# Performance work log

Hardware: AMD Instinct MI355X
Metric: run time of the kernel (lower is better)

Reference implementation:

```python
import jax, jax.numpy as jnp
import numpy as np

N_NODES = 100000
N_EDGES = 1600000
N_GRAPHS = 4096
IN_FEATS = 64
HIDDEN = 128


def setup_inputs() -> dict:
    key = jax.random.key(0)
    ks = jax.random.split(key, 16)
    feats_node = jax.random.normal(ks[0], (N_NODES, IN_FEATS), dtype=jnp.float32)
    feats_graph = jax.random.normal(ks[1], (N_GRAPHS, 3), dtype=jnp.float32)
    src = jax.random.randint(ks[2], (N_EDGES,), 0, N_NODES, dtype=jnp.int32)
    dst = jax.random.randint(ks[3], (N_EDGES,), 0, N_NODES, dtype=jnp.int32)
    node2graph = jnp.sort(jax.random.randint(ks[4], (N_NODES,), 0, N_GRAPHS, dtype=jnp.int32))
    # weights stored as [in, out] (torch Linear W.T); init per module: std=0.5 weights, bias ~ N(0.01, 0.001)
    def w(k, shape):
        return jax.random.normal(k, shape, dtype=jnp.float32) * 0.5
    def b(k, shape):
        return 0.01 + 0.001 * jax.random.normal(k, shape, dtype=jnp.float32)
    return {
        'feats_node': feats_node, 'feats_graph': feats_graph,
        'src': src, 'dst': dst, 'node2graph': node2graph,
        'W1': w(ks[5], (IN_FEATS, HIDDEN)), 'b1': b(ks[6], (HIDDEN,)),
        'W2': w(ks[7], (HIDDEN, HIDDEN)), 'b2': b(ks[8], (HIDDEN,)),
        'W3': w(ks[9], (HIDDEN, HIDDEN)), 'b3': b(ks[10], (HIDDEN,)),
        'L1w': w(ks[11], (HIDDEN + 3, 2 * HIDDEN)), 'L1b': b(ks[12], (2 * HIDDEN,)),
        'L2w': w(ks[13], (2 * HIDDEN, HIDDEN)), 'L2b': b(ks[14], (HIDDEN,)),
        'L3w': w(ks[15], (HIDDEN, 1)), 'L3b': b(jax.random.fold_in(key, 99), (1,)),
    }


def _graph_conv(x, W, b, src, dst, norm_out, norm_in):
    # DGL GraphConv(norm='both'): h_i = (sum_{j->i} x_j * d_out(j)^-1/2) * d_in(i)^-1/2 @ W + b
    m = (x * norm_out)[src]                       # [E, F] gather
    agg = jax.ops.segment_sum(m, dst, num_segments=N_NODES)
    return (agg * norm_in) @ W + b


def reference(feats_node, feats_graph, W1, b1, W2, b2, W3, b3, L1w, L1b, L2w, L2b, L3w, L3b, src, dst, node2graph):
    ones = jnp.ones((N_EDGES,), dtype=jnp.float32)
    deg_out = jax.ops.segment_sum(ones, src, num_segments=N_NODES)
    deg_in = jax.ops.segment_sum(ones, dst, num_segments=N_NODES)
    norm_out = jnp.clip(deg_out, 1.0, None)[:, None] ** -0.5  # [N,1]
    norm_in = jnp.clip(deg_in, 1.0, None)[:, None] ** -0.5

    x = jax.nn.selu(_graph_conv(feats_node, W1, b1, src, dst, norm_out, norm_in))
    x = jax.nn.selu(_graph_conv(x, W2, b2, src, dst, norm_out, norm_in))
    y_node = _graph_conv(x, W3, b3, src, dst, norm_out, norm_in)

    y_sum = jax.ops.segment_sum(y_node, node2graph, num_segments=N_GRAPHS)  # readout 'sum'
    y = jnp.concatenate([y_sum, feats_graph], axis=1)  # [G, H+3]
    y = jax.nn.selu(y @ L1w + L1b)
    y = jax.nn.selu(y @ L2w + L2b)
    return (y @ L3w + L3b).reshape(-1)
```

## Files before the change

### kernel.cpp

```cpp
#include <hip/hip_runtime.h>
#include <math.h>

#define SELU_ALPHA 1.6732632423543772f
#define SELU_SCALE 1.0507009873554805f

#define NBLK 512
#define MAXBKT 512

typedef __attribute__((ext_vector_type(8))) short bf16x8;
typedef __attribute__((ext_vector_type(4))) float f32x4;

__device__ __forceinline__ float selu_f(float x) {
    return SELU_SCALE * (x > 0.f ? x : SELU_ALPHA * expm1f(x));
}

__device__ __forceinline__ float bf2f(unsigned short u) {
    return __uint_as_float(((unsigned)u) << 16);
}
__device__ __forceinline__ unsigned short f2bf(float f) {
    unsigned u = __float_as_uint(f);
    unsigned r = (u + 0x7fffu + ((u >> 16) & 1u)) >> 16;
    return (unsigned short)r;
}

#define SCAN_B 1024

__global__ __launch_bounds__(256) void scan_block_sums(const int* __restrict__ in,
                                                       int* __restrict__ bsums, int n) {
    __shared__ int s[256];
    int b = blockIdx.x, t = threadIdx.x;
    int base = b * SCAN_B;
    int sum = 0;
    for (int i = t; i < SCAN_B; i += 256) {
        int idx = base + i;
        sum += (idx < n) ? in[idx] : 0;
    }
    s[t] = sum; __syncthreads();
    for (int off = 128; off > 0; off >>= 1) {
        if (t < off) s[t] += s[t + off];
        __syncthreads();
    }
    if (t == 0) bsums[b] = s[0];
}

__global__ __launch_bounds__(256) void scan_apply2(const int* __restrict__ in,
                                                   const int* __restrict__ bsums,
                                                   int* __restrict__ out, int n, int nb) {
    __shared__ int sb[512];
    __shared__ int s[256];
    __shared__ int blockoff;
    int b = blockIdx.x, t = threadIdx.x;

    int orig0 = (t < nb) ? bsums[t] : 0;
    int orig1 = (t + 256 < nb) ? bsums[t + 256] : 0;
    sb[t] = orig0; sb[t + 256] = orig1;
    __syncthreads();
    for (int off = 1; off < 512; off <<= 1) {
        int v0 = (t >= off) ? sb[t - off] : 0;
        int v1 = (t + 256 >= off) ? sb[t + 256 - off] : 0;
        __syncthreads();
        sb[t] += v0; sb[t + 256] += v1;
        __syncthreads();
    }
    if (t == (b & 255)) {
        bool hi = b >= 256;
        int incl = hi ? sb[t + 256] : sb[t];
        int orig = hi ? orig1 : orig0;
        blockoff = incl - orig;
    }
    __syncthreads();

    int idx0 = b * SCAN_B + t * 4;
    int v[4]; int tsum = 0;
    #pragma unroll
    for (int k = 0; k < 4; ++k) {
        int idx = idx0 + k;
        v[k] = (idx < n) ? in[idx] : 0;
        tsum += v[k];
    }
    s[t] = tsum; __syncthreads();
    for (int off = 1; off < 256; off <<= 1) {
        int x = (t >= off) ? s[t - off] : 0;
        __syncthreads();
        s[t] += x;
        __syncthreads();
    }
    int run = s[t] - tsum + blockoff;
    #pragma unroll
    for (int k = 0; k < 4; ++k) {
        int idx = idx0 + k;
        if (idx < n) out[idx] = run;
        run += v[k];
    }
}

__global__ __launch_bounds__(256) void hist_prep_kernel(
        const int* __restrict__ src, const int* __restrict__ dst,
        int* __restrict__ cntD, int* __restrict__ cntS, int E, int nbkt,
        const float* __restrict__ W1, const float* __restrict__ W2,
        const float* __restrict__ W3, const float* __restrict__ L1w,
        const float* __restrict__ L2w,
        unsigned short* __restrict__ Wt1, unsigned short* __restrict__ Wt2,
        unsigned short* __restrict__ Wt3, unsigned short* __restrict__ L1w16,
        unsigned short* __restrict__ L2w16) {
    if (blockIdx.x >= NBLK) {
        const int s0 = 128 * 64, s1 = 128 * 128, s2 = 128 * 128;
        const int s3 = 131 * 256 / 4, s4 = 256 * 128 / 4;
        int i = (blockIdx.x - NBLK) * 256 + threadIdx.x;
        if (i < s0) { int col = i / 64, k = i % 64; Wt1[i] = f2bf(W1[k * 128 + col]); return; }
        i -= s0;
        if (i < s1) { int col = i / 128, k = i % 128; Wt2[i] = f2bf(W2[k * 128 + col]); return; }
        i -= s1;
        if (i < s2) { int col = i / 128, k = i % 128; Wt3[i] = f2bf(W3[k * 128 + col]); return; }
        i -= s2;
        if (i < s3) {
            float4 v = reinterpret_cast<const float4*>(L1w)[i];
            unsigned short o[4] = { f2bf(v.x), f2bf(v.y), f2bf(v.z), f2bf(v.w) };
            reinterpret_cast<uint2*>(L1w16)[i] = *reinterpret_cast<uint2*>(o);
            return;
        }
        i -= s3;
        if (i < s4) {
            float4 v = reinterpret_cast<const float4*>(L2w)[i];
            unsigned short o[4] = { f2bf(v.x), f2bf(v.y), f2bf(v.z), f2bf(v.w) };
            reinterpret_cast<uint2*>(L2w16)[i] = *reinterpret_cast<uint2*>(o);
        }
        return;
    }
    __shared__ int hD[MAXBKT];
    __shared__ int hS[MAXBKT];
    int bb = blockIdx.x, t = threadIdx.x;
    for (int k = t; k < MAXBKT; k += 256) { hD[k] = 0; hS[k] = 0; }
    __syncthreads();
    int chunk = E / NBLK;
    int beg = bb * chunk, end = beg + chunk;
    for (int i = beg + t; i < end; i += 256) {
        atomicAdd(&hD[((unsigned)dst[i]) >> 8], 1);
        atomicAdd(&hS[((unsigned)src[i]) >> 8], 1);
    }
    __syncthreads();
    for (int k = t; k < nbkt; k += 256) {
        cntD[k * NBLK + bb] = hD[k];
        cntS[k * NBLK + bb] = hS[k];
    }
}

__global__ __launch_bounds__(256) void scatter_kernel(
        const int* __restrict__ src, const int* __restrict__ dst,
        const int* __restrict__ cntD, const int* __restrict__ cntS,
        unsigned* __restrict__ pairs, int* __restrict__ sbufm, int E, int nbkt) {
    __shared__ int cD[MAXBKT];
    __shared__ int cS[MAXBKT];
    int bb = blockIdx.x, t = threadIdx.x;
    for (int k = t; k < nbkt; k += 256) {
        cD[k] = cntD[k * NBLK + bb];
        cS[k] = cntS[k * NBLK + bb];
    }
    __syncthreads();
    int chunk = E / NBLK;
    int beg = bb * chunk, end = beg + chunk;
    for (int i = beg + t; i < end; i += 256) {
        unsigned s = (unsigned)src[i], d = (unsigned)dst[i];
        int pD = atomicAdd(&cD[d >> 8], 1);
        pairs[pD] = s | ((d & 255u) << 24);
        int pS = atomicAdd(&cS[s >> 8], 1);
        sbufm[pS] = (int)s;
    }
}

__global__ __launch_bounds__(256) void bucket_build_kernel(
        const int* __restrict__ sbufm, const unsigned* __restrict__ pairs,
        const int* __restrict__ cntD, const int* __restrict__ cntS,
        const float* __restrict__ feats,
        float* __restrict__ norm_out, unsigned short* __restrict__ feats16,
        int* __restrict__ row_start, int* __restrict__ deg_in,
        int* __restrict__ csr_src, int N, int E, int nbkt) {
    __shared__ int hist[256];
    __shared__ int sc[256];
    __shared__ int cur[256];
    __shared__ float nrm[256];
    int b = blockIdx.x, t = threadIdx.x;
    int node = (b << 8) + t;
    int node0 = b << 8;

    {
        int base = cntS[b * NBLK];
        int end = (b + 1 < nbkt) ? cntS[(b + 1) * NBLK] : 2 * E;
        hist[t] = 0; __syncthreads();
        for (int i = base + t; i < end; i += 256)
            atomicAdd(&hist[sbufm[i] & 255], 1);
        __syncthreads();
        float no = 1.f / sqrtf(fmaxf((float)hist[t], 1.f));
        nrm[t] = no;
        if (node < N) norm_out[node] = no;
        __syncthreads();
    }

    {
        int cnt = min(256, N - node0);
        for (int i = t; i < cnt * 8; i += 256) {
            int nl = i >> 3, c = i & 7;
            float no = nrm[nl];
            const float* fp = feats + (size_t)(node0 + nl) * 64 + c * 8;
            float4 a = *reinterpret_cast<const float4*>(fp);
            float4 bv = *reinterpret_cast<const float4*>(fp + 4);
            unsigned short o[8] = { f2bf(a.x * no), f2bf(a.y * no), f2bf(a.z * no), f2bf(a.w * no),
                                    f2bf(bv.x * no), f2bf(bv.y * no), f2bf(bv.z * no), f2bf(bv.w * no) };
            *reinterpret_cast<float4*>(feats16 + (size_t)(node0 + nl) * 64 + c * 8) =
                *reinterpret_cast<float4*>(o);
        }
        __syncthreads();
    }

    {
        int base = cntD[b * NBLK];
        int end = (b + 1 < nbkt) ? cntD[(b + 1) * NBLK] : E;
        hist[t] = 0; __syncthreads();
        for (int i = base + t; i < end; i += 256)
            atomicAdd(&hist[(pairs[i] >> 24) & 255], 1);
        __syncthreads();
        int v = hist[t];
        sc[t] = v; __syncthreads();
        for (int off = 1; off < 256; off <<= 1) {
            int x = (t >= off) ? sc[t - off] : 0;
            __syncthreads();
            sc[t] += x;
            __syncthreads();
        }
        int ex = sc[t] - v;
        cur[t] = base + ex;
        if (node < N) { row_start[node] = base + ex; deg_in[node] = v; }
        __syncthreads();
        for (int i = base + t; i < end; i += 256) {
            unsigned p = pairs[i];
            int pos = atomicAdd(&cur[(p >> 24) & 255], 1);
            csr_src[pos] = (int)(p & 0xFFFFFFu);
        }
    }
}

template<int TPG, int FIN>
__global__ __launch_bounds__(256) void csr_agg_kernel(
        const unsigned short* __restrict__ x, const int* __restrict__ row_start,
        const int* __restrict__ deg_in, const int* __restrict__ csr_src,
        unsigned short* __restrict__ agg, int N) {
    const int GPB = 256 / TPG;
    int g = threadIdx.x / TPG;
    int j = threadIdx.x % TPG;
    int n = blockIdx.x * GPB + g;
    if (n >= N) return;
    const int lane = threadIdx.x & 63;
    const int gbase = lane & ~(TPG - 1);
    int beg = row_start[n];
    int dg = deg_in[n];
    int end = beg + dg;
    float nin = 1.f / sqrtf(fmaxf((float)dg, 1.f));
    float acc[8] = {0.f, 0.f, 0.f, 0.f, 0.f, 0.f, 0.f, 0.f};
    int myIdx = (beg + j < end) ? csr_src[beg + j] : 0;
    for (int c = beg; c < end; c += TPG) {
        int cnt = end - c;
        int nxtIdx = (c + TPG + j < end) ? csr_src[c + TPG + j] : 0;
        float4 v[TPG];
        #pragma unroll
        for (int t = 0; t < TPG; ++t) {
            if (t < cnt) {
                int s = __shfl(myIdx, gbase + t, 64);
                v[t] = *reinterpret_cast<const float4*>(&x[(size_t)s * FIN + j * 8]);
            }
        }
        #pragma unroll
        for (int t = 0; t < TPG; ++t) {
            if (t < cnt) {
                const unsigned short* u = reinterpret_cast<const unsigned short*>(&v[t]);
                #pragma unroll
                for (int k = 0; k < 8; ++k) acc[k] += bf2f(u[k]);
            }
        }
        myIdx = nxtIdx;
    }
    unsigned short ov[8];
    #pragma unroll
    for (int k = 0; k < 8; ++k) ov[k] = f2bf(acc[k] * nin);
    *reinterpret_cast<float4*>(&agg[(size_t)n * FIN + j * 8]) = *reinterpret_cast<float4*>(ov);
}

template<int FIN, bool SELU, bool SCALE_OUT>
__global__ __launch_bounds__(256, 4) void gemm_mfma_kernel(
        const unsigned short* __restrict__ agg16,
        const unsigned short* __restrict__ Wt,
        const float* __restrict__ b,
        const float* __restrict__ norm_out,
        unsigned short* __restrict__ out,
        int N) {
    const int PAD = 8;
    const int LDW = FIN + PAD;
    const int CH = FIN / 8;
    __shared__ unsigned short sW[128 * LDW];
    const int tid = threadIdx.x;
    const int wave = tid >> 6, lane = tid & 63;
    const int wr = (wave >> 1) * 64;
    const int wc = (wave & 1) * 64;
    const int n0 = blockIdx.x * 128;

    for (int i = tid; i < 128 * CH; i += 256) {
        int col = i / CH, kc = i % CH;
        *reinterpret_cast<float4*>(&sW[col * LDW + kc * 8]) =
            *reinterpret_cast<const float4*>(&Wt[col * FIN + kc * 8]);
    }
    __syncthreads();

    const int l16 = lane & 15;
    const int lk = (lane >> 4) * 8;
    const bf16x8 zero8 = (bf16x8){0,0,0,0,0,0,0,0};
    f32x4 acc[4][4];
    #pragma unroll
    for (int mi = 0; mi < 4; ++mi)
        #pragma unroll
        for (int ci = 0; ci < 4; ++ci)
            acc[mi][ci] = (f32x4){0.f, 0.f, 0.f, 0.f};

    #pragma unroll
    for (int k0 = 0; k0 < FIN; k0 += 32) {
        bf16x8 a[4], w[4];
        #pragma unroll
        for (int mi = 0; mi < 4; ++mi) {
            int n = n0 + wr + mi * 16 + l16;
            a[mi] = (n < N)
                ? *reinterpret_cast<const bf16x8*>(&agg16[(size_t)n * FIN + k0 + lk])
                : zero8;
        }
        #pragma unroll
        for (int ci = 0; ci < 4; ++ci)
            w[ci] = *reinterpret_cast<const bf16x8*>(&sW[(wc + ci * 16 + l16) * LDW + k0 + lk]);
        #pragma unroll
        for (int mi = 0; mi < 4; ++mi)
            #pragma unroll
            for (int ci = 0; ci < 4; ++ci)
                acc[mi][ci] = __builtin_amdgcn_mfma_f32_16x16x32_bf16(
                    a[mi], w[ci], acc[mi][ci], 0, 0, 0);
    }

    const int rbase = (lane >> 4) * 4;
    #pragma unroll
    for (int ci = 0; ci < 4; ++ci) {
        int col = wc + ci * 16 + l16;
        float bias = b[col];
        #pragma unroll
        for (int mi = 0; mi < 4; ++mi) {
            #pragma unroll
            for (int r = 0; r < 4; ++r) {
                int n = n0 + wr + mi * 16 + rbase + r;
                if (n < N) {
                    float v = acc[mi][ci][r] + bias;
                    if (SELU) v = selu_f(v);
                    if (SCALE_OUT) v *= norm_out[n];
                    out[(size_t)n * 128 + col] = f2bf(v);
                }
            }
        }
    }
}

__global__ __launch_bounds__(128) void readout_kernel(
        const unsigned short* __restrict__ y, const int* __restrict__ n2g,
        float* __restrict__ gsum, int N, int G) {
    int g = blockIdx.x;
    int o = threadIdx.x;
    if (g >= G) return;
    int beg, end;
    {
        int lo = 0, hi = N;
        while (lo < hi) { int m = (lo + hi) >> 1; if (n2g[m] < g) lo = m + 1; else hi = m; }
        beg = lo;
        lo = beg; hi = N;
        while (lo < hi) { int m = (lo + hi) >> 1; if (n2g[m] < g + 1) lo = m + 1; else hi = m; }
        end = lo;
    }
    float acc = 0.f;
    for (int n = beg; n < end; ++n)
        acc += bf2f(y[(size_t)n * 128 + o]);
    gsum[(size_t)g * 128 + o] = acc;
}

__global__ __launch_bounds__(256) void mlp1_kernel(
        const float* __restrict__ gsum, const float* __restrict__ fg,
        const unsigned short* __restrict__ W16,
        const float* __restrict__ b,
        float* __restrict__ y1, int G) {
    __shared__ unsigned short sW[131 * 256];
    __shared__ float sIn[16][132];
    int tid = threadIdx.x;
    for (int i = tid; i < 131 * 256 / 2; i += 256)
        reinterpret_cast<unsigned*>(sW)[i] = reinterpret_cast<const unsigned*>(W16)[i];
    int g0 = blockIdx.x * 16;
    for (int i = tid; i < 16 * 131; i += 256) {
        int g = i / 131, k = i - g * 131;
        float v = 0.f;
        if (g0 + g < G)
            v = (k < 128) ? gsum[(size_t)(g0 + g) * 128 + k]
                          : fg[(size_t)(g0 + g) * 3 + (k - 128)];
        sIn[g][k] = v;
    }
    __syncthreads();
    float bias = b[tid];
    for (int g = 0; g < 16; ++g) {
        if (g0 + g >= G) break;
        float acc = bias;
        #pragma unroll 8
        for (int k = 0; k < 131; ++k)
            acc += sIn[g][k] * bf2f(sW[k * 256 + tid]);
        y1[(size_t)(g0 + g) * 256 + tid] = selu_f(acc);
    }
}

__global__ __launch_bounds__(256) void mlp23_kernel(
        const float* __restrict__ y1,
        const unsigned short* __restrict__ W16,
        const float* __restrict__ b2v,
        const float* __restrict__ L3w,
        const float* __restrict__ L3b,
        float* __restrict__ out, int G) {
    __shared__ unsigned short sW[256 * 128];
    __shared__ float sIn[16][256];
    __shared__ float sL3[128];
    __shared__ float red[16][2];
    int tid = threadIdx.x;
    for (int i = tid; i < 256 * 128 / 2; i += 256)
        reinterpret_cast<unsigned*>(sW)[i] = reinterpret_cast<const unsigned*>(W16)[i];
    if (tid < 128) sL3[tid] = L3w[tid];
    int g0 = blockIdx.x * 16;
    for (int i = tid; i < 16 * 256; i += 256) {
        int g = i >> 8, k = i & 255;
        sIn[g][k] = (g0 + g < G) ? y1[(size_t)(g0 + g) * 256 + k] : 0.f;
    }
    __syncthreads();
    int o = tid & 127;
    int half = tid >> 7;
    int lane = tid & 63;
    int wv = tid >> 6;
    float bias = b2v[o];
    float w3 = sL3[o];
    for (int gg = 0; gg < 8; ++gg) {
        int g = half * 8 + gg;
        float acc = bias;
        #pragma unroll 8
        for (int k = 0; k < 256; ++k)
            acc += sIn[g][k] * bf2f(sW[k * 128 + o]);
        float v = selu_f(acc) * w3;
        #pragma unroll
        for (int off = 32; off > 0; off >>= 1)
            v += __shfl_down(v, off, 64);
        if (lane == 0) red[g][wv & 1] = v;
    }
    __syncthreads();
    if (tid < 16) {
        int g = g0 + tid;
        if (g < G) out[g] = red[tid][0] + red[tid][1] + L3b[0];
    }
}

extern "C" void kernel_launch(void* const* d_in, const int* in_sizes, int n_in,
                              void* d_out, int out_size, void* d_ws, size_t ws_size,
                              hipStream_t stream) {
    const float* feats_node  = (const float*)d_in[0];
    const float* feats_graph = (const float*)d_in[1];
    const int*   src         = (const int*)d_in[2];
    const int*   dst         = (const int*)d_in[3];
    const int*   node2graph  = (const int*)d_in[4];
    const float* W1 = (const float*)d_in[5];
    const float* b1 = (const float*)d_in[6];
    const float* W2 = (const float*)d_in[7];
    const float* b2 = (const float*)d_in[8];
    const float* W3 = (const float*)d_in[9];
    const float* b3 = (const float*)d_in[10];
    const float* L1w = (const float*)d_in[11];
    const float* L1b = (const float*)d_in[12];
    const float* L2w = (const float*)d_in[13];
    const float* L2b = (const float*)d_in[14];
    const float* L3w = (const float*)d_in[15];
    const float* L3b = (const float*)d_in[16];

    const int N = in_sizes[0] / 64;
    const int G = in_sizes[1] / 3;
    const int E = in_sizes[2];
    const int NBKT = (N + 255) >> 8;
    const int nmat = NBKT * NBLK;
    const int nscan = 2 * nmat;
    const int NBsc = (nscan + SCAN_B - 1) / SCAN_B;

    int* iws = (int*)d_ws;
    int* deg_in_i  = iws;
    int* row_start = deg_in_i + N;
    int* bsums     = row_start + N;
    int* cntD      = bsums + 512;
    int* cntS      = cntD + nmat;
    int* csr_src   = cntS + nmat;

    float* norm_out = (float*)(csr_src + E);

    unsigned short* feats16 = (unsigned short*)(norm_out + N);
    unsigned short* x16     = feats16 + (size_t)N * 64;
    unsigned short* agg16   = x16 + (size_t)N * 128;
    unsigned short* y16     = agg16 + (size_t)N * 128;
    unsigned short* Wt1     = y16 + (size_t)N * 128;
    unsigned short* Wt2     = Wt1 + 128 * 64;
    unsigned short* Wt3     = Wt2 + 128 * 128;
    unsigned short* L1w16   = Wt3 + 128 * 128;
    unsigned short* L2w16   = L1w16 + 131 * 256;

    float* gsum = (float*)(L2w16 + 256 * 128);
    float* y1   = gsum + (size_t)G * 128;

    unsigned* pairs = (unsigned*)(((uintptr_t)y16 + 15) & ~(uintptr_t)15);
    int*      sbuf  = (int*)(pairs + E);
    int*      sbufm = sbuf - E;

    float* out = (float*)d_out;

    {
        const int wtotal = 128 * 64 + 2 * 128 * 128 + 131 * 256 / 4 + 256 * 128 / 4;
        const int wblocks = (wtotal + 255) / 256;
        hist_prep_kernel<<<NBLK + wblocks, 256, 0, stream>>>(
            src, dst, cntD, cntS, E, NBKT,
            W1, W2, W3, L1w, L2w, Wt1, Wt2, Wt3, L1w16, L2w16);
    }

    scan_block_sums<<<NBsc, 256, 0, stream>>>(cntD, bsums, nscan);
    scan_apply2<<<NBsc, 256, 0, stream>>>(cntD, bsums, cntD, nscan, NBsc);
    scatter_kernel<<<NBLK, 256, 0, stream>>>(src, dst, cntD, cntS, pairs, sbufm, E, NBKT);

    bucket_build_kernel<<<NBKT, 256, 0, stream>>>(
        sbufm, pairs, cntD, cntS, feats_node,
        norm_out, feats16, row_start, deg_in_i, csr_src, N, E, NBKT);

    const int gemm_grid = (N + 127) / 128;

    csr_agg_kernel<8, 64><<<(N + 31) / 32, 256, 0, stream>>>(
        feats16, row_start, deg_in_i, csr_src, agg16, N);
    gemm_mfma_kernel<64, true, true><<<gemm_grid, 256, 0, stream>>>(
        agg16, Wt1, b1, norm_out, x16, N);

    csr_agg_kernel<16, 128><<<(N + 15) / 16, 256, 0, stream>>>(
        x16, row_start, deg_in_i, csr_src, agg16, N);
    gemm_mfma_kernel<128, true, true><<<gemm_grid, 256, 0, stream>>>(
        agg16, Wt2, b2, norm_out, x16, N);

    csr_agg_kernel<16, 128><<<(N + 15) / 16, 256, 0, stream>>>(
        x16, row_start, deg_in_i, csr_src, agg16, N);
    gemm_mfma_kernel<128, false, false><<<gemm_grid, 256, 0, stream>>>(
        agg16, Wt3, b3, norm_out, y16, N);

    readout_kernel<<<G, 128, 0, stream>>>(y16, node2graph, gsum, N, G);

    mlp1_kernel<<<(G + 15) / 16, 256, 0, stream>>>(gsum, feats_graph, L1w16, L1b, y1, G);
    mlp23_kernel<<<(G + 15) / 16, 256, 0, stream>>>(
        y1, L2w16, L2b, L3w, L3b, out, G);
}
```

Baseline: 416.9 us.

## Fold layer-3 weight and bias into the first MLP layer algebraically

The third graph-conv layer has no activation before the sum readout and the first MLP linear layer, so W3 is folded into L1w and b3 is turned into a per-graph node-count term. The layer-3 GEMM over all nodes is removed, and readout sums the normalized aggregate directly. In exchange, prep does a small 128x128x256 matmul and the weights and agg16 are rounded to bf16 at different points, which can shift numerics slightly.

```diff
diff --git a/kernel.cpp b/kernel.cpp
--- a/kernel.cpp
+++ b/kernel.cpp
@@ -98,29 +98,49 @@
         const int* __restrict__ src, const int* __restrict__ dst,
         int* __restrict__ cntD, int* __restrict__ cntS, int E, int nbkt,
         const float* __restrict__ W1, const float* __restrict__ W2,
-        const float* __restrict__ W3, const float* __restrict__ L1w,
-        const float* __restrict__ L2w,
+        const float* __restrict__ W3, const float* __restrict__ b3,
+        const float* __restrict__ L1w, const float* __restrict__ L2w,
         unsigned short* __restrict__ Wt1, unsigned short* __restrict__ Wt2,
-        unsigned short* __restrict__ Wt3, unsigned short* __restrict__ L1w16,
-        unsigned short* __restrict__ L2w16) {
+        unsigned short* __restrict__ W1c, unsigned short* __restrict__ L2w16) {
     if (blockIdx.x >= NBLK) {
-        const int s0 = 128 * 64, s1 = 128 * 128, s2 = 128 * 128;
-        const int s3 = 131 * 256 / 4, s4 = 256 * 128 / 4;
+        const int s0 = 128 * 64;
+        const int s1 = 128 * 128;
+        const int s2 = 128 * 256;
+        const int s3 = 3 * 256;
+        const int s4 = 256;
+        const int s5 = 256 * 128 / 4;
         int i = (blockIdx.x - NBLK) * 256 + threadIdx.x;
         if (i < s0) { int col = i / 64, k = i % 64; Wt1[i] = f2bf(W1[k * 128 + col]); return; }
         i -= s0;
         if (i < s1) { int col = i / 128, k = i % 128; Wt2[i] = f2bf(W2[k * 128 + col]); return; }
         i -= s1;
-        if (i < s2) { int col = i / 128, k = i % 128; Wt3[i] = f2bf(W3[k * 128 + col]); return; }
+        if (i < s2) {
+            int k = i >> 8, o = i & 255;
+            float acc = 0.f;
+            #pragma unroll 8
+            for (int m = 0; m < 128; ++m)
+                acc += W3[k * 128 + m] * L1w[m * 256 + o];
+            W1c[k * 256 + o] = f2bf(acc);
+            return;
+        }
         i -= s2;
         if (i < s3) {
-            float4 v = reinterpret_cast<const float4*>(L1w)[i];
-            unsigned short o[4] = { f2bf(v.x), f2bf(v.y), f2bf(v.z), f2bf(v.w) };
-            reinterpret_cast<uint2*>(L1w16)[i] = *reinterpret_cast<uint2*>(o);
+            int r = i >> 8, o = i & 255;
+            W1c[(128 + r) * 256 + o] = f2bf(L1w[(128 + r) * 256 + o]);
             return;
         }
         i -= s3;
         if (i < s4) {
+            int o = i;
+            float acc = 0.f;
+            #pragma unroll 8
+            for (int m = 0; m < 128; ++m)
+                acc += b3[m] * L1w[m * 256 + o];
+            W1c[131 * 256 + o] = f2bf(acc);
+            return;
+        }
+        i -= s4;
+        if (i < s5) {
             float4 v = reinterpret_cast<const float4*>(L2w)[i];
             unsigned short o[4] = { f2bf(v.x), f2bf(v.y), f2bf(v.z), f2bf(v.w) };
             reinterpret_cast<uint2*>(L2w16)[i] = *reinterpret_cast<uint2*>(o);
@@ -363,7 +383,7 @@
 
 __global__ __launch_bounds__(128) void readout_kernel(
         const unsigned short* __restrict__ y, const int* __restrict__ n2g,
-        float* __restrict__ gsum, int N, int G) {
+        float* __restrict__ gsum, float* __restrict__ cntf, int N, int G) {
     int g = blockIdx.x;
     int o = threadIdx.x;
     if (g >= G) return;
@@ -380,25 +400,29 @@
     for (int n = beg; n < end; ++n)
         acc += bf2f(y[(size_t)n * 128 + o]);
     gsum[(size_t)g * 128 + o] = acc;
+    if (o == 0) cntf[g] = (float)(end - beg);
 }
 
 __global__ __launch_bounds__(256) void mlp1_kernel(
         const float* __restrict__ gsum, const float* __restrict__ fg,
-        const unsigned short* __restrict__ W16,
+        const float* __restrict__ cntf,
+        const unsigned short* __restrict__ W1c,
         const float* __restrict__ b,
         float* __restrict__ y1, int G) {
-    __shared__ unsigned short sW[131 * 256];
+    __shared__ unsigned short sW[132 * 256];
     __shared__ float sIn[16][132];
     int tid = threadIdx.x;
-    for (int i = tid; i < 131 * 256 / 2; i += 256)
-        reinterpret_cast<unsigned*>(sW)[i] = reinterpret_cast<const unsigned*>(W16)[i];
+    for (int i = tid; i < 132 * 256 / 2; i += 256)
+        reinterpret_cast<unsigned*>(sW)[i] = reinterpret_cast<const unsigned*>(W1c)[i];
     int g0 = blockIdx.x * 16;
-    for (int i = tid; i < 16 * 131; i += 256) {
-        int g = i / 131, k = i - g * 131;
+    for (int i = tid; i < 16 * 132; i += 256) {
+        int g = i / 132, k = i - g * 132;
         float v = 0.f;
-        if (g0 + g < G)
-            v = (k < 128) ? gsum[(size_t)(g0 + g) * 128 + k]
-                          : fg[(size_t)(g0 + g) * 3 + (k - 128)];
+        if (g0 + g < G) {
+            if (k < 128)       v = gsum[(size_t)(g0 + g) * 128 + k];
+            else if (k < 131)  v = fg[(size_t)(g0 + g) * 3 + (k - 128)];
+            else               v = cntf[g0 + g];
+        }
         sIn[g][k] = v;
     }
     __syncthreads();
@@ -406,8 +430,8 @@
     for (int g = 0; g < 16; ++g) {
         if (g0 + g >= G) break;
         float acc = bias;
-        #pragma unroll 8
-        for (int k = 0; k < 131; ++k)
+        #pragma unroll 4
+        for (int k = 0; k < 132; ++k)
             acc += sIn[g][k] * bf2f(sW[k * 256 + tid]);
         y1[(size_t)(g0 + g) * 256 + tid] = selu_f(acc);
     }
@@ -501,28 +525,27 @@
     unsigned short* feats16 = (unsigned short*)(norm_out + N);
     unsigned short* x16     = feats16 + (size_t)N * 64;
     unsigned short* agg16   = x16 + (size_t)N * 128;
-    unsigned short* y16     = agg16 + (size_t)N * 128;
-    unsigned short* Wt1     = y16 + (size_t)N * 128;
+    unsigned short* Wt1     = agg16 + (size_t)N * 128;
     unsigned short* Wt2     = Wt1 + 128 * 64;
-    unsigned short* Wt3     = Wt2 + 128 * 128;
-    unsigned short* L1w16   = Wt3 + 128 * 128;
-    unsigned short* L2w16   = L1w16 + 131 * 256;
+    unsigned short* W1c     = Wt2 + 128 * 128;
+    unsigned short* L2w16   = W1c + 132 * 256;
 
     float* gsum = (float*)(L2w16 + 256 * 128);
-    float* y1   = gsum + (size_t)G * 128;
-
-    unsigned* pairs = (unsigned*)(((uintptr_t)y16 + 15) & ~(uintptr_t)15);
+    float* cntf = gsum + (size_t)G * 128;
+    float* y1   = cntf + G;
+
+    unsigned* pairs = (unsigned*)(((uintptr_t)agg16 + 15) & ~(uintptr_t)15);
     int*      sbuf  = (int*)(pairs + E);
     int*      sbufm = sbuf - E;
 
     float* out = (float*)d_out;
 
     {
-        const int wtotal = 128 * 64 + 2 * 128 * 128 + 131 * 256 / 4 + 256 * 128 / 4;
+        const int wtotal = 128 * 64 + 128 * 128 + 128 * 256 + 3 * 256 + 256 + 256 * 128 / 4;
         const int wblocks = (wtotal + 255) / 256;
         hist_prep_kernel<<<NBLK + wblocks, 256, 0, stream>>>(
             src, dst, cntD, cntS, E, NBKT,
-            W1, W2, W3, L1w, L2w, Wt1, Wt2, Wt3, L1w16, L2w16);
+            W1, W2, W3, b3, L1w, L2w, Wt1, Wt2, W1c, L2w16);
     }
 
     scan_block_sums<<<NBsc, 256, 0, stream>>>(cntD, bsums, nscan);
@@ -547,12 +570,11 @@
 
     csr_agg_kernel<16, 128><<<(N + 15) / 16, 256, 0, stream>>>(
         x16, row_start, deg_in_i, csr_src, agg16, N);
-    gemm_mfma_kernel<128, false, false><<<gemm_grid, 256, 0, stream>>>(
-        agg16, Wt3, b3, norm_out, y16, N);
-
-    readout_kernel<<<G, 128, 0, stream>>>(y16, node2graph, gsum, N, G);
-
-    mlp1_kernel<<<(G + 15) / 16, 256, 0, stream>>>(gsum, feats_graph, L1w16, L1b, y1, G);
+
+    readout_kernel<<<G, 128, 0, stream>>>(agg16, node2graph, gsum, cntf, N, G);
+
+    mlp1_kernel<<<(G + 15) / 16, 256, 0, stream>>>(
+        gsum, feats_graph, cntf, W1c, L1b, y1, G);
     mlp23_kernel<<<(G + 15) / 16, 256, 0, stream>>>(
         y1, L2w16, L2b, L3w, L3b, out, G);
 }
```

After: 390.8 us. 1.07x faster.
